# Kernel optimization log

Measured on AMD Instinct MI355X. Metric: run time of the kernel, lower is better.

## Reference

```python
import jax, jax.numpy as jnp
import numpy as np
from jax import lax

T = 36          # sequence length
N_POLES = 80    # N -> dictionary has 2N+1 = 161 atoms
LAM = 0.1       # lam_f
MAX_ITER = 100
TOL = 1e-05


def real_D(T, rho, theta):
    # CONSTR=True: squash rho into [0.001, 1.15], theta into [0, pi]
    rmin, rmax = 0.001, 1.15
    r = rmin + (rmax - rmin) * jax.nn.sigmoid(rho)          # (N,)
    th = jnp.pi * jax.nn.sigmoid(theta)                     # (N,)
    i = jnp.arange(T, dtype=rho.dtype)[:, None]             # (T,1)
    p = r[None, :] ** i                                     # (T,N)
    W1 = p * jnp.cos(i * th[None, :])
    W2 = p * jnp.sin(i * th[None, :])
    D = jnp.concatenate([jnp.ones((T, 1), rho.dtype), W1, W2], axis=1)  # (T, 2N+1)
    # NORM=True: column-normalize all but the constant column
    norms = jnp.linalg.norm(D[:, 1:], axis=0, keepdims=True)
    return jnp.concatenate([D[:, :1], D[:, 1:] / norms], axis=1)


def softshrink(v, thr):
    return jnp.sign(v) * jnp.maximum(jnp.abs(v) - thr, 0.0)


def fista_efc(D, Y, lam, max_iter):
    # argmin_C ||Y - D C||_2^2 + lam |C|_1
    DtD = D.T @ D                                           # (P,P)
    L_inv = 1.0 / jnp.linalg.norm(DtD, ord=2)               # 1/spectral norm
    P = DtD.shape[0]
    dim_data = Y.shape[-1]
    A = jnp.eye(P, dtype=Y.dtype) - L_inv * DtD             # (P,P)
    B = L_inv * jnp.einsum('tp,btd->bpd', D, Y)             # (B,P,d)
    thr = lax.stop_gradient(lam * L_inv)                    # .item() in torch => constant

    batch = Y.shape[0]
    x0 = jnp.zeros((batch, P, dim_data), Y.dtype)
    y0 = jnp.zeros((batch, P, dim_data), Y.dtype)

    def body(carry, _):
        x, y, t, done = carry
        x_new = softshrink(jnp.einsum('pq,bqd->bpd', A, y) + B, thr)
        diff = jnp.linalg.norm(x - x_new) / dim_data        # Frobenius over all elems
        t_new = (1.0 + jnp.sqrt(1.0 + 4.0 * t * t)) / 2.0
        tt = (t - 1.0) / t_new
        y_new = (1.0 + tt) * x_new - tt * x
        # if already converged before this step, freeze the state (early return)
        x_out = jnp.where(done, x, x_new)
        y_out = jnp.where(done, y, y_new)
        t_out = jnp.where(done, t, t_new)
        done_new = done | (diff < TOL)
        return (x_out, y_out, t_out, done_new), None

    init = (x0, y0, jnp.float32(1.0), jnp.bool_(False))
    (x_fin, _, _, _), _ = lax.scan(body, init, None, length=max_iter)
    return x_fin


def reference(x, rho, theta):
    # DAN.forward with wiRH=False, freezeD=False
    dic = real_D(T, rho, theta)                             # (T, 2N+1)
    C = fista_efc(dic, x, LAM, MAX_ITER)                    # (B, 2N+1, d)
    reconst = jnp.einsum('tp,bpd->btd', dic, C)             # (B, T, d)
    return C, dic, reconst


def setup_inputs() -> dict:
    key = jax.random.key(0)
    k1, k2, k3 = jax.random.split(key, 3)
    x = jax.random.normal(k1, (256, T, 50), dtype=jnp.float32)
    rho = jax.random.uniform(k2, (N_POLES,), dtype=jnp.float32)
    theta = jax.random.uniform(k3, (N_POLES,), dtype=jnp.float32)
    return {"x": x, "rho": rho, "theta": theta}
```

## Files before the change

kernel.cpp:

```cpp
#include <hip/hip_runtime.h>
#include <math.h>

typedef _Float16 half_t;
typedef __attribute__((ext_vector_type(8))) _Float16 half8;
typedef __attribute__((ext_vector_type(4))) _Float16 half4;
typedef __attribute__((ext_vector_type(4))) float floatx4;

#define TDIM 36
#define PDIM 161
#define NCOL 50
#define NITER 100
#define PITER8 50

#define NKA 5
#define GSTR 44
#define SPS 196

#define YROW 384
#define RROW 128

#define SWZ(row, byteoff) ((byteoff) ^ (((row) & 7) << 4))

#define BY_Y    0
#define BY_R    24576
#define BY_LRTH 28672
#define BY_Y0   32768
#define BY_SC   33024
#define BY_GS   33040
#define BY_G2   39376
#define BY_G4   45712
#define LDS_TOTAL 52048

#define MFMA16 __builtin_amdgcn_mfma_f32_16x16x32_f16

__global__ __launch_bounds__(768, 3)
void dan_kernel(const float* __restrict__ xin, const float* __restrict__ rho,
                const float* __restrict__ theta, float* __restrict__ outC,
                float* __restrict__ outDic, float* __restrict__ outR)
{
  extern __shared__ char smc[];
  float*  sc   = (float*)(smc + BY_SC);
  float*  Gs   = (float*)(smc + BY_GS);
  float*  G2   = (float*)(smc + BY_G2);
  float*  G4   = (float*)(smc + BY_G4);
  float*  Y0f  = (float*)(smc + BY_Y0);
  float*  Df   = (float*)(smc + BY_Y);
  float*  lrth = (float*)(smc + BY_LRTH);

  const int tid = threadIdx.x;
  const int b = blockIdx.x;
  const int wave = tid >> 6, lane = tid & 63;
  const int q = lane >> 4, ln = lane & 15;

  {
    unsigned int* z = (unsigned int*)smc;
    for (int i = tid; i < LDS_TOTAL / 4; i += 768) z[i] = 0u;
  }
  __syncthreads();

  if (tid >= 1 && tid < PDIM) {
    const bool is_sin = tid > 80;
    const int n = is_sin ? (tid - 81) : (tid - 1);
    lrth[tid]       = logf(0.001f + 1.149f / (1.0f + expf(-rho[n])));
    lrth[161 + tid] = 3.14159265358979f / (1.0f + expf(-theta[n]));
  }
  __syncthreads();

  for (int i = tid; i < TDIM * PDIM; i += 768) {
    const int t = i / PDIM, p = i - t * PDIM;
    float val;
    if (p == 0) {
      val = 1.0f;
    } else {
      const float ft = (float)t;
      const float e = expf(ft * lrth[p]);
      const float ang = ft * lrth[161 + p];
      val = e * (p > 80 ? sinf(ang) : cosf(ang));
    }
    Df[t * SPS + p] = val;
  }
  __syncthreads();

  if (tid >= 1 && tid < PDIM) {
    float s2 = 0.0f;
    for (int t = 0; t < TDIM; ++t) {
      const float v = Df[t * SPS + tid];
      s2 += v * v;
    }
    const float inv = 1.0f / sqrtf(s2);
    for (int t = 0; t < TDIM; ++t) Df[t * SPS + tid] *= inv;
  }
  __syncthreads();

  if (tid < 666) {
    int i = 0, rem = tid;
    while (rem >= TDIM - i) { rem -= TDIM - i; ++i; }
    const int j = i + rem;
    const float4* ri = (const float4*)(Df + i * SPS);
    const float4* rj = (const float4*)(Df + j * SPS);
    float a = 0.0f;
    #pragma unroll 7
    for (int k = 0; k < SPS / 4; ++k) {
      const float4 x = ri[k], y = rj[k];
      a += x.x * y.x + x.y * y.y + x.z * y.z + x.w * y.w;
    }
    Gs[i * GSTR + j] = a;
    Gs[j * GSTR + i] = a;
  }
  if (b == 0) {
    for (int i = tid; i < TDIM * PDIM; i += 768) {
      const int t = i / PDIM, p = i - t * PDIM;
      outDic[i] = Df[t * SPS + p];
    }
  }

  const int mtA = wave >> 2;
  const int ntA = wave & 3;
  const int pgrp = wave >> 2;
  const int npt = (pgrp == 0) ? 4 : 3;

  half8 DhF[NKA], DlF[NKA];
  {
    const int row = 16 * mtA + ln;
    #pragma unroll
    for (int ks = 0; ks < NKA; ++ks) {
      half8 hh, ll;
      #pragma unroll
      for (int e = 0; e < 8; ++e) {
        const int p = 32 * ks + 8 * q + e + 1;
        const float v = (row < TDIM) ? Df[row * SPS + p] : 0.0f;
        const half_t h = (half_t)v;
        hh[e] = h;
        ll[e] = (half_t)(v - (float)h);
      }
      DhF[ks] = hh;
      DlF[ks] = ll;
    }
  }
  half8 DtH[4][2], DtL[4][2];
  #pragma unroll
  for (int k = 0; k < 4; ++k) {
    if (k < npt) {
      const int atom = 16 * (pgrp + 3 * k) + ln + 1;
      #pragma unroll
      for (int ks = 0; ks < 2; ++ks) {
        half8 hh, ll;
        #pragma unroll
        for (int e = 0; e < 8; ++e) {
          const int t = 32 * ks + 8 * q + e;
          const float v = (t < TDIM) ? Df[t * SPS + atom] : 0.0f;
          const half_t h = (half_t)v;
          hh[e] = h;
          ll[e] = (half_t)(v - (float)h);
        }
        DtH[k][ks] = hh;
        DtL[k][ks] = ll;
      }
    }
  }
  float yA[4];
  {
    const float* xb = xin + b * TDIM * NCOL;
    const int c = 16 * ntA + ln;
    #pragma unroll
    for (int r = 0; r < 4; ++r) {
      const int t = 16 * mtA + 4 * q + r;
      yA[r] = (t < TDIM && c < NCOL) ? xb[t * NCOL + c] : 0.0f;
    }
  }
  __syncthreads();

  if (tid < 666) {
    int i = 0, rem = tid;
    while (rem >= TDIM - i) { rem -= TDIM - i; ++i; }
    const int j = i + rem;
    const float4* ri = (const float4*)(Gs + i * GSTR);
    const float4* rj = (const float4*)(Gs + j * GSTR);
    float a = 0.0f;
    #pragma unroll
    for (int k = 0; k < GSTR / 4; ++k) {
      const float4 x = ri[k], y = rj[k];
      a += x.x * y.x + x.y * y.y + x.z * y.z + x.w * y.w;
    }
    G2[i * GSTR + j] = a;
    G2[j * GSTR + i] = a;
  }
  __syncthreads();
  if (tid < 666) {
    int i = 0, rem = tid;
    while (rem >= TDIM - i) { rem -= TDIM - i; ++i; }
    const int j = i + rem;
    const float4* ri = (const float4*)(G2 + i * GSTR);
    const float4* rj = (const float4*)(G2 + j * GSTR);
    float a = 0.0f;
    #pragma unroll
    for (int k = 0; k < GSTR / 4; ++k) {
      const float4 x = ri[k], y = rj[k];
      a += x.x * y.x + x.y * y.y + x.z * y.z + x.w * y.w;
    }
    G4[i * GSTR + j] = a;
    G4[j * GSTR + i] = a;
  }
  __syncthreads();
  if (tid < 666) {
    int i = 0, rem = tid;
    while (rem >= TDIM - i) { rem -= TDIM - i; ++i; }
    const int j = i + rem;
    const float4* ri = (const float4*)(G4 + i * GSTR);
    const float4* rj = (const float4*)(G4 + j * GSTR);
    float a = 0.0f;
    #pragma unroll
    for (int k = 0; k < GSTR / 4; ++k) {
      const float4 x = ri[k], y = rj[k];
      a += x.x * y.x + x.y * y.y + x.z * y.z + x.w * y.w;
    }
    G2[i * GSTR + j] = a;
    G2[j * GSTR + i] = a;
  }
  __syncthreads();

  if (wave == 0) {
    float g8r[36];
    #pragma unroll
    for (int j = 0; j < 36; ++j) g8r[j] = (lane < 36) ? G2[lane * GSTR + j] : 0.0f;
    float v = (lane < 36) ? 1.0f : 0.0f;
    for (int it = 0; it < PITER8; ++it) {
      const int vi = __float_as_int(v);
      float w0 = 0.0f, w1 = 0.0f, w2 = 0.0f, w3 = 0.0f;
      #pragma unroll
      for (int j = 0; j < 36; j += 4) {
        w0 = fmaf(g8r[j],     __int_as_float(__builtin_amdgcn_readlane(vi, j)),     w0);
        w1 = fmaf(g8r[j + 1], __int_as_float(__builtin_amdgcn_readlane(vi, j + 1)), w1);
        w2 = fmaf(g8r[j + 2], __int_as_float(__builtin_amdgcn_readlane(vi, j + 2)), w2);
        w3 = fmaf(g8r[j + 3], __int_as_float(__builtin_amdgcn_readlane(vi, j + 3)), w3);
      }
      float w = (w0 + w1) + (w2 + w3);
      float s = w * w;
      #pragma unroll
      for (int off = 32; off > 0; off >>= 1) s += __shfl_xor(s, off, 64);
      v = w * rsqrtf(s);
    }
    const int vi = __float_as_int(v);
    float w0 = 0.0f, w1 = 0.0f;
    #pragma unroll
    for (int j = 0; j < 36; j += 2) {
      const float gi0 = (lane < 36) ? Gs[lane * GSTR + j]     : 0.0f;
      const float gi1 = (lane < 36) ? Gs[lane * GSTR + j + 1] : 0.0f;
      w0 = fmaf(gi0, __int_as_float(__builtin_amdgcn_readlane(vi, j)),     w0);
      w1 = fmaf(gi1, __int_as_float(__builtin_amdgcn_readlane(vi, j + 1)), w1);
    }
    float num = v * (w0 + w1);
    #pragma unroll
    for (int off = 32; off > 0; off >>= 1) num += __shfl_xor(num, off, 64);
    if (lane == 0) {
      sc[0] = 1.0f / num;
      sc[1] = 0.1f / num;
    }
  } else {
    unsigned int* z = (unsigned int*)smc;
    for (int i = tid - 64; i < BY_SC / 4; i += 704) z[i] = 0u;
  }
  __syncthreads();
  const float L_inv = sc[0];
  const float thr = sc[1];

  float xR[4][4], yR[4][4];
  #pragma unroll
  for (int k = 0; k < 4; ++k)
    #pragma unroll
    for (int r = 0; r < 4; ++r) { xR[k][r] = 0.0f; yR[k][r] = 0.0f; }
  float x0v = 0.0f, y0v = 0.0f;

  float tk = 1.0f;

  for (int it = 0; it < NITER; ++it) {
    {
      const int n0 = 16 * ntA + ln;
      const float y0c = Y0f[n0];
      floatx4 aH0 = {0.f,0.f,0.f,0.f}, aH1 = {0.f,0.f,0.f,0.f};
      floatx4 aL0 = {0.f,0.f,0.f,0.f}, aL1 = {0.f,0.f,0.f,0.f};
      const char* yrow = smc + BY_Y + n0 * YROW;
      #pragma unroll
      for (int ks = 0; ks < NKA; ++ks) {
        const int kb = (32 * ks + 8 * q) * 2;
        const half8 b0 = *(const half8*)(yrow + SWZ(n0, kb));
        if (ks & 1) {
          aH1 = MFMA16(DhF[ks], b0, aH1, 0, 0, 0);
          aL1 = MFMA16(DlF[ks], b0, aL1, 0, 0, 0);
        } else {
          aH0 = MFMA16(DhF[ks], b0, aH0, 0, 0, 0);
          aL0 = MFMA16(DlF[ks], b0, aL0, 0, 0, 0);
        }
      }
      const int t0 = 16 * mtA + 4 * q;
      half4 hv;
      #pragma unroll
      for (int r = 0; r < 4; ++r)
        hv[r] = (half_t)(yA[r] - y0c - ((aH0[r] + aH1[r]) + (aL0[r] + aL1[r])));
      *(half4*)(smc + BY_R + n0 * RROW + SWZ(n0, t0 * 2)) = hv;
    }
    __syncthreads();

    const float tnew = 0.5f * (1.0f + sqrtf(1.0f + 4.0f * tk * tk));
    const float ttf = (tk - 1.0f) / tnew;
    tk = tnew;

    {
      const int c = 16 * ntA + ln;
      const char* rrow = smc + BY_R + c * RROW;
      const half8 rb0 = *(const half8*)(rrow + SWZ(c, 16 * q));
      const half8 rb1 = *(const half8*)(rrow + SWZ(c, 64 + 16 * q));

      if (pgrp == 1) {
        float s0 = 0.0f;
        #pragma unroll
        for (int e = 0; e < 8; ++e) s0 += (float)rb0[e];
        float s1 = 0.0f;
        #pragma unroll
        for (int e = 0; e < 4; ++e) s1 += (float)rb1[e];
        float part = s0 + (q == 0 ? s1 : 0.0f);
        part += __shfl_xor(part, 16, 64);
        part += __shfl_xor(part, 32, 64);
        const float w = y0v + L_inv * part;
        const float cl = fminf(fmaxf(w, -thr), thr);
        const float xn = w - cl;
        const float yn = xn + ttf * (xn - x0v);
        x0v = xn;
        y0v = yn;
        if (q == 0) Y0f[c] = yn;
      }

      #pragma unroll
      for (int k = 0; k < 4; ++k) {
        if (k < npt) {
          floatx4 a = {0.f,0.f,0.f,0.f};
          a = MFMA16(DtH[k][0], rb0, a, 0, 0, 0);
          a = MFMA16(DtL[k][0], rb0, a, 0, 0, 0);
          a = MFMA16(DtH[k][1], rb1, a, 0, 0, 0);
          a = MFMA16(DtL[k][1], rb1, a, 0, 0, 0);
          const int s0_ = 16 * (pgrp + 3 * k) + 4 * q;
          half4 hv;
          #pragma unroll
          for (int r = 0; r < 4; ++r) {
            const float w = yR[k][r] + L_inv * a[r];
            const float cl = fminf(fmaxf(w, -thr), thr);
            const float xn = w - cl;
            const float yn = xn + ttf * (xn - xR[k][r]);
            xR[k][r] = xn;
            yR[k][r] = yn;
            hv[r] = (half_t)yn;
          }
          *(half4*)(smc + BY_Y + c * YROW + SWZ(c, s0_ * 2)) = hv;
        }
      }
    }
    __syncthreads();
  }

  float* Cb = outC + b * PDIM * NCOL;
  {
    const int c = 16 * ntA + ln;
    if (c < NCOL) {
      #pragma unroll
      for (int k = 0; k < 4; ++k) {
        if (k < npt) {
          const int pbase = 16 * (pgrp + 3 * k) + 4 * q + 1;
          #pragma unroll
          for (int r = 0; r < 4; ++r)
            Cb[(pbase + r) * NCOL + c] = xR[k][r];
        }
      }
      if (pgrp == 1 && q == 0) Cb[c] = x0v;
    }
  }
  {
    const int c = 16 * ntA + ln;
    #pragma unroll
    for (int k = 0; k < 4; ++k) {
      if (k < npt) {
        const int s0_ = 16 * (pgrp + 3 * k) + 4 * q;
        half4 hv;
        #pragma unroll
        for (int r = 0; r < 4; ++r) hv[r] = (half_t)xR[k][r];
        *(half4*)(smc + BY_Y + c * YROW + SWZ(c, s0_ * 2)) = hv;
      }
    }
    if (pgrp == 1 && q == 0) Y0f[c] = x0v;
  }
  __syncthreads();
  {
    const int n0 = 16 * ntA + ln;
    const float x0c = Y0f[n0];
    floatx4 aH0 = {0.f,0.f,0.f,0.f}, aH1 = {0.f,0.f,0.f,0.f};
    floatx4 aL0 = {0.f,0.f,0.f,0.f}, aL1 = {0.f,0.f,0.f,0.f};
    const char* yrow = smc + BY_Y + n0 * YROW;
    #pragma unroll
    for (int ks = 0; ks < NKA; ++ks) {
      const int kb = (32 * ks + 8 * q) * 2;
      const half8 b0 = *(const half8*)(yrow + SWZ(n0, kb));
      if (ks & 1) {
        aH1 = MFMA16(DhF[ks], b0, aH1, 0, 0, 0);
        aL1 = MFMA16(DlF[ks], b0, aL1, 0, 0, 0);
      } else {
        aH0 = MFMA16(DhF[ks], b0, aH0, 0, 0, 0);
        aL0 = MFMA16(DlF[ks], b0, aL0, 0, 0, 0);
      }
    }
    float* Rb = outR + b * TDIM * NCOL;
    const int c = n0;
    if (c < NCOL) {
      const int t0 = 16 * mtA + 4 * q;
      #pragma unroll
      for (int r = 0; r < 4; ++r) {
        const int t = t0 + r;
        if (t < TDIM)
          Rb[t * NCOL + c] = x0c + (aH0[r] + aH1[r]) + (aL0[r] + aL1[r]);
      }
    }
  }
}


extern "C" void kernel_launch(void* const* d_in, const int* in_sizes, int n_in,
                              void* d_out, int out_size, void* d_ws, size_t ws_size,
                              hipStream_t stream) {
  const float* x     = (const float*)d_in[0];
  const float* rho   = (const float*)d_in[1];
  const float* theta = (const float*)d_in[2];

  float* out    = (float*)d_out;
  float* outC   = out;
  float* outDic = out + 256 * PDIM * NCOL;
  float* outR   = outDic + TDIM * PDIM;

  hipLaunchKernelGGL(dan_kernel, dim3(256), dim3(768), LDS_TOTAL, stream,
                     x, rho, theta, outC, outDic, outR);
}
```

Baseline: 239.3 us.

## Remap phase-two wave tiling so each wave handles two column tiles per atom tile

Restructures the D^T·R update so each of the 12 waves owns up to two atom tiles and two column tiles, instead of one column tile and three or four atom tiles. The D^T fragments held in registers shrink, and each fragment is reused across two column tiles. The constant-atom update moves to wave group 5, and residual rows beyond T are explicitly written as zero. This trades fewer register-resident D^T fragments for more LDS reads of residuals per wave, and it changes load balance, since some waves now get only one atom tile.

```diff
diff --git a/kernel.cpp b/kernel.cpp
--- a/kernel.cpp
+++ b/kernel.cpp
@@ -116,8 +116,8 @@
 
   const int mtA = wave >> 2;
   const int ntA = wave & 3;
-  const int pgrp = wave >> 2;
-  const int npt = (pgrp == 0) ? 4 : 3;
+  const int g = wave >> 1;
+  const int h = wave & 1;
 
   half8 DhF[NKA], DlF[NKA];
   {
@@ -129,19 +129,20 @@
       for (int e = 0; e < 8; ++e) {
         const int p = 32 * ks + 8 * q + e + 1;
         const float v = (row < TDIM) ? Df[row * SPS + p] : 0.0f;
-        const half_t h = (half_t)v;
-        hh[e] = h;
-        ll[e] = (half_t)(v - (float)h);
+        const half_t h2 = (half_t)v;
+        hh[e] = h2;
+        ll[e] = (half_t)(v - (float)h2);
       }
       DhF[ks] = hh;
       DlF[ks] = ll;
     }
   }
-  half8 DtH[4][2], DtL[4][2];
+  half8 DtH[2][2], DtL[2][2];
   #pragma unroll
-  for (int k = 0; k < 4; ++k) {
-    if (k < npt) {
-      const int atom = 16 * (pgrp + 3 * k) + ln + 1;
+  for (int k = 0; k < 2; ++k) {
+    const int pt = g + 6 * k;
+    if (pt < 10) {
+      const int atom = 16 * pt + ln + 1;
       #pragma unroll
       for (int ks = 0; ks < 2; ++ks) {
         half8 hh, ll;
@@ -149,9 +150,9 @@
         for (int e = 0; e < 8; ++e) {
           const int t = 32 * ks + 8 * q + e;
           const float v = (t < TDIM) ? Df[t * SPS + atom] : 0.0f;
-          const half_t h = (half_t)v;
-          hh[e] = h;
-          ll[e] = (half_t)(v - (float)h);
+          const half_t h2 = (half_t)v;
+          hh[e] = h2;
+          ll[e] = (half_t)(v - (float)h2);
         }
         DtH[k][ks] = hh;
         DtL[k][ks] = ll;
@@ -264,11 +265,13 @@
   const float L_inv = sc[0];
   const float thr = sc[1];
 
-  float xR[4][4], yR[4][4];
+  float xR[2][2][4], yR[2][2][4];
   #pragma unroll
-  for (int k = 0; k < 4; ++k)
-    #pragma unroll
-    for (int r = 0; r < 4; ++r) { xR[k][r] = 0.0f; yR[k][r] = 0.0f; }
+  for (int k = 0; k < 2; ++k)
+    #pragma unroll
+    for (int s = 0; s < 2; ++s)
+      #pragma unroll
+      for (int r = 0; r < 4; ++r) { xR[k][s][r] = 0.0f; yR[k][s][r] = 0.0f; }
   float x0v = 0.0f, y0v = 0.0f;
 
   float tk = 1.0f;
@@ -293,10 +296,12 @@
         }
       }
       const int t0 = 16 * mtA + 4 * q;
+      const bool tval = (t0 < TDIM);
       half4 hv;
       #pragma unroll
       for (int r = 0; r < 4; ++r)
-        hv[r] = (half_t)(yA[r] - y0c - ((aH0[r] + aH1[r]) + (aL0[r] + aL1[r])));
+        hv[r] = tval ? (half_t)(yA[r] - y0c - ((aH0[r] + aH1[r]) + (aL0[r] + aL1[r])))
+                     : (half_t)0.0f;
       *(half4*)(smc + BY_R + n0 * RROW + SWZ(n0, t0 * 2)) = hv;
     }
     __syncthreads();
@@ -306,51 +311,63 @@
     tk = tnew;
 
     {
-      const int c = 16 * ntA + ln;
-      const char* rrow = smc + BY_R + c * RROW;
-      const half8 rb0 = *(const half8*)(rrow + SWZ(c, 16 * q));
-      const half8 rb1 = *(const half8*)(rrow + SWZ(c, 64 + 16 * q));
-
-      if (pgrp == 1) {
-        float s0 = 0.0f;
+      half8 rb[2][2];
+      #pragma unroll
+      for (int s = 0; s < 2; ++s) {
+        const int cS = 16 * (2 * h + s) + ln;
+        const char* rrow = smc + BY_R + cS * RROW;
+        rb[s][0] = *(const half8*)(rrow + SWZ(cS, 16 * q));
+        rb[s][1] = *(const half8*)(rrow + SWZ(cS, 64 + 16 * q));
+      }
+
+      if (g == 5) {
+        float p0 = 0.0f, p1 = 0.0f;
         #pragma unroll
-        for (int e = 0; e < 8; ++e) s0 += (float)rb0[e];
-        float s1 = 0.0f;
-        #pragma unroll
-        for (int e = 0; e < 4; ++e) s1 += (float)rb1[e];
-        float part = s0 + (q == 0 ? s1 : 0.0f);
-        part += __shfl_xor(part, 16, 64);
-        part += __shfl_xor(part, 32, 64);
-        const float w = y0v + L_inv * part;
-        const float cl = fminf(fmaxf(w, -thr), thr);
-        const float xn = w - cl;
-        const float yn = xn + ttf * (xn - x0v);
-        x0v = xn;
-        y0v = yn;
-        if (q == 0) Y0f[c] = yn;
-      }
-
-      #pragma unroll
-      for (int k = 0; k < 4; ++k) {
-        if (k < npt) {
-          floatx4 a = {0.f,0.f,0.f,0.f};
-          a = MFMA16(DtH[k][0], rb0, a, 0, 0, 0);
-          a = MFMA16(DtL[k][0], rb0, a, 0, 0, 0);
-          a = MFMA16(DtH[k][1], rb1, a, 0, 0, 0);
-          a = MFMA16(DtL[k][1], rb1, a, 0, 0, 0);
-          const int s0_ = 16 * (pgrp + 3 * k) + 4 * q;
-          half4 hv;
+        for (int e = 0; e < 8; ++e) {
+          p0 += (float)rb[0][0][e] + (float)rb[0][1][e];
+          p1 += (float)rb[1][0][e] + (float)rb[1][1][e];
+        }
+        p0 += __shfl_xor(p0, 16, 64);  p0 += __shfl_xor(p0, 32, 64);
+        p1 += __shfl_xor(p1, 16, 64);  p1 += __shfl_xor(p1, 32, 64);
+        if (q < 2) {
+          const float part = (q & 1) ? p1 : p0;
+          const int cSel = 16 * (2 * h + (q & 1)) + ln;
+          const float w = y0v + L_inv * part;
+          const float cl = fminf(fmaxf(w, -thr), thr);
+          const float xn = w - cl;
+          const float yn = xn + ttf * (xn - x0v);
+          x0v = xn;
+          y0v = yn;
+          Y0f[cSel] = yn;
+        }
+      }
+
+      #pragma unroll
+      for (int k = 0; k < 2; ++k) {
+        const int pt = g + 6 * k;
+        if (pt < 10) {
           #pragma unroll
-          for (int r = 0; r < 4; ++r) {
-            const float w = yR[k][r] + L_inv * a[r];
-            const float cl = fminf(fmaxf(w, -thr), thr);
-            const float xn = w - cl;
-            const float yn = xn + ttf * (xn - xR[k][r]);
-            xR[k][r] = xn;
-            yR[k][r] = yn;
-            hv[r] = (half_t)yn;
+          for (int s = 0; s < 2; ++s) {
+            floatx4 a = {0.f,0.f,0.f,0.f};
+            a = MFMA16(DtH[k][0], rb[s][0], a, 0, 0, 0);
+            a = MFMA16(DtL[k][0], rb[s][0], a, 0, 0, 0);
+            a = MFMA16(DtH[k][1], rb[s][1], a, 0, 0, 0);
+            a = MFMA16(DtL[k][1], rb[s][1], a, 0, 0, 0);
+            const int cS = 16 * (2 * h + s) + ln;
+            const int s0_ = 16 * pt + 4 * q;
+            half4 hv;
+            #pragma unroll
+            for (int r = 0; r < 4; ++r) {
+              const float w = yR[k][s][r] + L_inv * a[r];
+              const float cl = fminf(fmaxf(w, -thr), thr);
+              const float xn = w - cl;
+              const float yn = xn + ttf * (xn - xR[k][s][r]);
+              xR[k][s][r] = xn;
+              yR[k][s][r] = yn;
+              hv[r] = (half_t)yn;
+            }
+            *(half4*)(smc + BY_Y + cS * YROW + SWZ(cS, s0_ * 2)) = hv;
           }
-          *(half4*)(smc + BY_Y + c * YROW + SWZ(c, s0_ * 2)) = hv;
         }
       }
     }
@@ -358,34 +375,43 @@
   }
 
   float* Cb = outC + b * PDIM * NCOL;
-  {
-    const int c = 16 * ntA + ln;
-    if (c < NCOL) {
-      #pragma unroll
-      for (int k = 0; k < 4; ++k) {
-        if (k < npt) {
-          const int pbase = 16 * (pgrp + 3 * k) + 4 * q + 1;
+  #pragma unroll
+  for (int k = 0; k < 2; ++k) {
+    const int pt = g + 6 * k;
+    if (pt < 10) {
+      #pragma unroll
+      for (int s = 0; s < 2; ++s) {
+        const int cS = 16 * (2 * h + s) + ln;
+        if (cS < NCOL) {
           #pragma unroll
           for (int r = 0; r < 4; ++r)
-            Cb[(pbase + r) * NCOL + c] = xR[k][r];
-        }
-      }
-      if (pgrp == 1 && q == 0) Cb[c] = x0v;
-    }
-  }
-  {
-    const int c = 16 * ntA + ln;
-    #pragma unroll
-    for (int k = 0; k < 4; ++k) {
-      if (k < npt) {
-        const int s0_ = 16 * (pgrp + 3 * k) + 4 * q;
+            Cb[(16 * pt + 4 * q + r + 1) * NCOL + cS] = xR[k][s][r];
+        }
+      }
+    }
+  }
+  if (g == 5 && q < 2) {
+    const int cSel = 16 * (2 * h + (q & 1)) + ln;
+    if (cSel < NCOL) Cb[cSel] = x0v;
+  }
+  #pragma unroll
+  for (int k = 0; k < 2; ++k) {
+    const int pt = g + 6 * k;
+    if (pt < 10) {
+      #pragma unroll
+      for (int s = 0; s < 2; ++s) {
+        const int cS = 16 * (2 * h + s) + ln;
+        const int s0_ = 16 * pt + 4 * q;
         half4 hv;
         #pragma unroll
-        for (int r = 0; r < 4; ++r) hv[r] = (half_t)xR[k][r];
-        *(half4*)(smc + BY_Y + c * YROW + SWZ(c, s0_ * 2)) = hv;
-      }
-    }
-    if (pgrp == 1 && q == 0) Y0f[c] = x0v;
+        for (int r = 0; r < 4; ++r) hv[r] = (half_t)xR[k][s][r];
+        *(half4*)(smc + BY_Y + cS * YROW + SWZ(cS, s0_ * 2)) = hv;
+      }
+    }
+  }
+  if (g == 5 && q < 2) {
+    const int cSel = 16 * (2 * h + (q & 1)) + ln;
+    Y0f[cSel] = x0v;
   }
   __syncthreads();
   {
```

Result: slower. 245.9 us (+2.7%).
